# Performance work log

Measured on AMD Instinct MI355X. Metric: run time of the kernel, lower is better.

## Reference

```python
import jax, jax.numpy as jnp
import numpy as np

EMBED_DIM = 1024
NUM_HEADS = 16
MICRO_HEADS = 8
HEAD_DIM = EMBED_DIM // NUM_HEADS
N_BLOCKS = NUM_HEADS // MICRO_HEADS
B, N = 2, 2048


def setup_inputs() -> dict:
    key = jax.random.key(0)
    ks = jax.random.split(key, 9)
    s = 1.0 / np.sqrt(EMBED_DIM)
    return {
        "x": jax.random.normal(ks[0], (B, N, EMBED_DIM), dtype=jnp.float32),
        "Wq": jax.random.uniform(ks[1], (EMBED_DIM, EMBED_DIM), jnp.float32, -s, s),
        "bq": jax.random.uniform(ks[2], (EMBED_DIM,), jnp.float32, -s, s),
        "Wk": jax.random.uniform(ks[3], (EMBED_DIM, EMBED_DIM), jnp.float32, -s, s),
        "bk": jax.random.uniform(ks[4], (EMBED_DIM,), jnp.float32, -s, s),
        "Wv": jax.random.uniform(ks[5], (EMBED_DIM, EMBED_DIM), jnp.float32, -s, s),
        "bv": jax.random.uniform(ks[6], (EMBED_DIM,), jnp.float32, -s, s),
        "Wo": jax.random.uniform(ks[7], (EMBED_DIM, EMBED_DIM), jnp.float32, -s, s),
        "bo": jax.random.uniform(ks[8], (EMBED_DIM,), jnp.float32, -s, s),
    }


def _scramble(t, b, n):
    # Replicates torch's Qh[:, :, hs:he, :].contiguous().view(B*mh, N, dh)
    # which is a raw row-major reshape mixing (N, mh) -> (mh, N) per batch.
    # (B, N, E) -> (B, N, nb, mh, dh) -> (B, nb, N, mh, dh) -> raw reshape -> (B, nb, mh, N, dh)
    t = t.reshape(b, n, N_BLOCKS, MICRO_HEADS, HEAD_DIM)
    t = jnp.transpose(t, (0, 2, 1, 3, 4))
    return t.reshape(b, N_BLOCKS, MICRO_HEADS, n, HEAD_DIM)


def reference(x, Wq, bq, Wk, bk, Wv, bv, Wo, bo):
    b, n, e = x.shape
    scale = HEAD_DIM ** -0.5
    Q = x @ Wq.T + bq
    K = x @ Wk.T + bk
    V = x @ Wv.T + bv
    q = _scramble(Q, b, n)  # (B, nb, mh, N, dh)
    k = _scramble(K, b, n)
    v = _scramble(V, b, n)
    s = jnp.einsum("bgmqd,bgmkd->bgmqk", q, k) * scale  # (B, nb, mh, N, N)
    causal = jnp.tril(jnp.ones((n, n), dtype=bool))
    s = jnp.where(causal, s, -jnp.inf)
    p = jax.nn.softmax(s, axis=-1)
    ctx = jnp.einsum("bgmqk,bgmkd->bgmqd", p, v)  # (B, nb, mh, N, dh)
    # inverse raw reshape: (mh, N, dh) -> (N, mh*dh) per (b, g), then concat blocks
    ctx = ctx.reshape(b, N_BLOCKS, n, MICRO_HEADS * HEAD_DIM)
    ctx = jnp.transpose(ctx, (0, 2, 1, 3)).reshape(b, n, e)
    return ctx @ Wo.T + bo
```

## Files before the change

### kernel.cpp

```cpp
#include <hip/hip_runtime.h>
#include <hip/hip_bf16.h>


typedef unsigned short ushortT;
typedef __attribute__((ext_vector_type(8))) short short8;
typedef __attribute__((ext_vector_type(4))) float floatx4;

__device__ inline float bf2f(ushortT u) {
    union { unsigned int i; float f; } v; v.i = ((unsigned int)u) << 16; return v.f;
}
__device__ inline ushortT f2bf(float f) {
    union { float f; unsigned int i; } v; v.f = f;
    unsigned int x = v.i;
    return (ushortT)((x + 0x7fffu + ((x >> 16) & 1u)) >> 16);
}

__device__ inline void gl_lds16(const ushortT* g, ushortT* lds) {
    __builtin_amdgcn_global_load_lds(
        (const __attribute__((address_space(1))) unsigned int*)g,
        (__attribute__((address_space(3))) unsigned int*)lds, 16, 0, 0);
}

__global__ __launch_bounds__(256) void cvt_bf16(
    const float* __restrict__ x,
    const float* __restrict__ Wq, const float* __restrict__ Wk,
    const float* __restrict__ Wv, const float* __restrict__ Wo,
    ushortT* __restrict__ xb, ushortT* __restrict__ Wb)
{
    const unsigned tid = blockIdx.x * 256 + threadIdx.x;
    const size_t e = (size_t)tid * 8;
    const float* src;
    ushortT* dst;
    size_t off;
    if (e < (size_t)(4u << 20)) { src = x; dst = xb; off = e; }
    else {
        const size_t r = e - (size_t)(4u << 20);
        const int wsel = (int)(r >> 20);
        off = r & 0xFFFFFu;
        src = (wsel == 0) ? Wq : (wsel == 1) ? Wk : (wsel == 2) ? Wv : Wo;
        dst = Wb + ((size_t)wsel << 20);
    }
    const float4 f0 = ((const float4*)(src + off))[0];
    const float4 f1 = ((const float4*)(src + off))[1];
    union { __hip_bfloat162 h[4]; uint4 u; } pk;
    pk.h[0] = __float22bfloat162_rn(float2{f0.x, f0.y});
    pk.h[1] = __float22bfloat162_rn(float2{f0.z, f0.w});
    pk.h[2] = __float22bfloat162_rn(float2{f1.x, f1.y});
    pk.h[3] = __float22bfloat162_rn(float2{f1.z, f1.w});
    *(uint4*)(dst + off) = pk.u;
}

template <bool OUT_F32>
__global__ __launch_bounds__(256) void gemm_lds(
    const ushortT* __restrict__ A, const ushortT* __restrict__ Wst,
    const float* __restrict__ b0, const float* __restrict__ b1, const float* __restrict__ b2,
    void* __restrict__ O0, void* __restrict__ O1, void* __restrict__ O2)
{
    __shared__ __align__(16) ushortT As[128 * 64];
    __shared__ __align__(16) ushortT Bs[128 * 64];
    const int t = threadIdx.x;
    const int m0 = blockIdx.y * 128;
    const int n0g = blockIdx.x * 128;
    const int mat = n0g >> 10;
    const int n0 = n0g & 1023;
    const ushortT* W = Wst + ((size_t)mat << 20);
    const float* bias = (mat == 0) ? b0 : (mat == 1) ? b1 : b2;
    void* Out        = (mat == 0) ? O0 : (mat == 1) ? O1 : O2;

    const int w = t >> 6, lane = t & 63;
    const int wm = w >> 1, wn = w & 1;
    const int col16 = lane & 15, quad = lane >> 4;

    floatx4 acc[4][4];
    for (int i = 0; i < 4; i++)
        for (int j = 0; j < 4; j++) acc[i][j] = (floatx4)0.0f;

    const int cid0 = w * 256 + lane;

    for (int k0 = 0; k0 < 1024; k0 += 64) {
        #pragma unroll
        for (int q = 0; q < 4; q++) {
            const int cid = cid0 + q * 64;
            const int row = cid >> 3;
            const int sch = (cid & 7) ^ (row & 7);
            ushortT* dstA = As + (size_t)(w * 256 + q * 64) * 8;
            ushortT* dstB = Bs + (size_t)(w * 256 + q * 64) * 8;
            gl_lds16(A + (size_t)(m0 + row) * 1024 + k0 + sch * 8, dstA);
            gl_lds16(W + (size_t)(n0 + row) * 1024 + k0 + sch * 8, dstB);
        }
        __syncthreads();
        #pragma unroll
        for (int ks = 0; ks < 64; ks += 32) {
            const int cbase = (ks >> 3) + quad;
            const int sw = col16 & 7;
            short8 a[4], b[4];
            #pragma unroll
            for (int i = 0; i < 4; i++) {
                const int row = wm * 64 + i * 16 + col16;
                a[i] = *(const short8*)(As + row * 64 + ((cbase ^ sw) << 3));
            }
            #pragma unroll
            for (int j = 0; j < 4; j++) {
                const int row = wn * 64 + j * 16 + col16;
                b[j] = *(const short8*)(Bs + row * 64 + ((cbase ^ sw) << 3));
            }
            #pragma unroll
            for (int i = 0; i < 4; i++)
                #pragma unroll
                for (int j = 0; j < 4; j++)
                    acc[i][j] = __builtin_amdgcn_mfma_f32_16x16x32_bf16(b[j], a[i], acc[i][j], 0, 0, 0);
        }
        __syncthreads();
    }

    #pragma unroll
    for (int i = 0; i < 4; i++) {
        const int m = m0 + wm * 64 + i * 16 + col16;
        #pragma unroll
        for (int j = 0; j < 4; j++) {
            const int nb = n0 + wn * 64 + j * 16 + quad * 4;
            const float4 bv4 = *(const float4*)(bias + nb);
            const float v0 = acc[i][j][0] + bv4.x;
            const float v1 = acc[i][j][1] + bv4.y;
            const float v2 = acc[i][j][2] + bv4.z;
            const float v3 = acc[i][j][3] + bv4.w;
            if constexpr (OUT_F32) {
                *(float4*)((float*)Out + (size_t)m * 1024 + nb) = float4{v0, v1, v2, v3};
            } else {
                union { __hip_bfloat162 h[2]; unsigned long long u; } pk2;
                pk2.h[0] = __float22bfloat162_rn(float2{v0, v1});
                pk2.h[1] = __float22bfloat162_rn(float2{v2, v3});
                *(unsigned long long*)((ushortT*)Out + (size_t)m * 1024 + nb) = pk2.u;
            }
        }
    }
}

__global__ __launch_bounds__(256) void transpose_v(
    const ushortT* __restrict__ Vb, ushortT* __restrict__ VT)
{
    __shared__ ushortT L[64 * 65];
    const int bid = blockIdx.x;
    const int pt = bid & 31, s = bid >> 5;
    const int bb = s >> 4, g = (s >> 3) & 1, mh = s & 7;
    const size_t baseoff = (size_t)bb * 2048 * 1024 + (size_t)g * 512;
    const int t = threadIdx.x;
    {
        const int pr = t >> 2, seg = t & 3;
        const int i = mh * 2048 + pt * 64 + pr;
        const uint4* src = (const uint4*)(Vb + baseoff + (size_t)(i >> 3) * 1024 + (i & 7) * 64 + seg * 16);
        union { uint4 u[2]; ushortT h[16]; } tmp;
        tmp.u[0] = src[0]; tmp.u[1] = src[1];
        #pragma unroll
        for (int d = 0; d < 16; d++) L[pr * 65 + seg * 16 + d] = tmp.h[d];
    }
    __syncthreads();
    {
        const int dc = t >> 2, pseg = t & 3;
        union { uint4 u[2]; ushortT h[16]; } tmp;
        #pragma unroll
        for (int j = 0; j < 16; j++) tmp.h[j] = L[(pseg * 16 + j) * 65 + dc];
        uint4* dst = (uint4*)(VT + (size_t)s * 64 * 2048 + (size_t)dc * 2048 + pt * 64 + pseg * 16);
        dst[0] = tmp.u[0]; dst[1] = tmp.u[1];
    }
}

__global__ __launch_bounds__(256) void attn(
    const ushortT* __restrict__ Qb, const ushortT* __restrict__ Kb,
    const ushortT* __restrict__ VT, ushortT* __restrict__ Cb)
{
    __shared__ __align__(16) ushortT Ks[2][64 * 64];
    __shared__ __align__(16) ushortT Vs[2][64 * 64];
    __shared__ __align__(16) ushortT Ps[64 * 64];

    const int t = threadIdx.x;
    const int bid = blockIdx.x;
    const int xcd = bid & 7;
    const int jj  = bid >> 3;
    const int s   = xcd * 4 + (jj >> 4);
    const int p   = jj & 15;
    const int qtA = p, qtB = 31 - p;
    const int bb = s >> 4, g = (s >> 3) & 1, mh = s & 7;

    const int w = t >> 6, lane = t & 63;
    const int col16 = lane & 15, quad = lane >> 4;

    const size_t baseoff = (size_t)bb * 2048 * 1024 + (size_t)g * 512;
    const size_t vtbase  = (size_t)s * 64 * 2048;
    const int i0A = mh * 2048 + qtA * 64;
    const int i0B = mh * 2048 + qtB * 64;
    const int qloc = w * 16 + col16;
    const int psw = qloc & 7;
    const float KL = 0.125f * 1.44269504f;

    short8 qreg[2][2];
    {
        const int iA = i0A + qloc, iB = i0B + qloc;
        const ushortT* pA = Qb + baseoff + (size_t)(iA >> 3) * 1024 + (iA & 7) * 64;
        const ushortT* pB = Qb + baseoff + (size_t)(iB >> 3) * 1024 + (iB & 7) * 64;
        qreg[0][0] = *(const short8*)(pA + quad * 8);
        qreg[0][1] = *(const short8*)(pA + 32 + quad * 8);
        qreg[1][0] = *(const short8*)(pB + quad * 8);
        qreg[1][1] = *(const short8*)(pB + 32 + quad * 8);
    }

    auto stageKV = [&](int kt, int bsel) {
        ushortT* kd = &Ks[bsel][0] + (size_t)(w * 128) * 8;
        ushortT* vd = &Vs[bsel][0] + (size_t)(w * 128) * 8;
        #pragma unroll
        for (int q = 0; q < 2; q++) {
            const int cid = w * 128 + q * 64 + lane;
            const int row = cid >> 3;
            const int sch = (cid & 7) ^ (row & 7);
            const int jr = mh * 2048 + kt * 64 + row;
            gl_lds16(Kb + baseoff + (size_t)(jr >> 3) * 1024 + (jr & 7) * 64 + sch * 8,
                     kd + q * 64 * 8);
            gl_lds16(VT + vtbase + (size_t)row * 2048 + kt * 64 + sch * 8,
                     vd + q * 64 * 8);
        }
    };

    float l_s[2] = {0.f, 0.f};
    floatx4 Oacc[2][4];
    for (int tl = 0; tl < 2; tl++)
        for (int c = 0; c < 4; c++) Oacc[tl][c] = (floatx4)0.0f;

    stageKV(0, 0);
    const int ktmax = qtB;
    for (int kt = 0; kt <= ktmax; ++kt) {
        const int bsel = kt & 1;
        __syncthreads();
        if (kt < ktmax) stageKV(kt + 1, bsel ^ 1);

        #pragma unroll
        for (int tile = 0; tile < 2; ++tile) {
            const int qt = tile ? qtB : qtA;
            if (kt > qt) continue;

            floatx4 sc[4];
            for (int c = 0; c < 4; c++) sc[c] = (floatx4)0.0f;
            #pragma unroll
            for (int ks = 0; ks < 64; ks += 32) {
                const short8 bq = qreg[tile][ks >> 5];
                #pragma unroll
                for (int c = 0; c < 4; c++) {
                    const int krow = c * 16 + col16;
                    const short8 ak = *(const short8*)(&Ks[bsel][0] + krow * 64 +
                                        ((((ks >> 3) + quad) ^ (krow & 7)) << 3));
                    sc[c] = __builtin_amdgcn_mfma_f32_16x16x32_bf16(ak, bq, sc[c], 0, 0, 0);
                }
            }

            if (kt == qt) {
                #pragma unroll
                for (int c = 0; c < 4; c++)
                    #pragma unroll
                    for (int r = 0; r < 4; r++)
                        if ((c * 16 + quad * 4 + r) > qloc) sc[c][r] = -1e30f;
            }

            float lsum = l_s[tile];
            #pragma unroll
            for (int c = 0; c < 4; c++) {
                #pragma unroll
                for (int r = 0; r < 4; r++) {
                    const float pv = exp2f(sc[c][r] * KL);
                    sc[c][r] = pv;
                    lsum += pv;
                }
                const int key0 = c * 16 + quad * 4;
                union { __hip_bfloat162 h[2]; unsigned long long u; } pk2;
                pk2.h[0] = __float22bfloat162_rn(float2{sc[c][0], sc[c][1]});
                pk2.h[1] = __float22bfloat162_rn(float2{sc[c][2], sc[c][3]});
                *(unsigned long long*)(Ps + qloc * 64 +
                    (((key0 >> 3) ^ psw) << 3) + (key0 & 7)) = pk2.u;
            }
            l_s[tile] = lsum;

            #pragma unroll
            for (int kk = 0; kk < 64; kk += 32) {
                const short8 bp = *(const short8*)(Ps + qloc * 64 +
                                    ((((kk >> 3) + quad) ^ psw) << 3));
                #pragma unroll
                for (int c = 0; c < 4; c++) {
                    const int drow = c * 16 + col16;
                    const short8 av = *(const short8*)(&Vs[bsel][0] + drow * 64 +
                                        ((((kk >> 3) + quad) ^ (drow & 7)) << 3));
                    Oacc[tile][c] = __builtin_amdgcn_mfma_f32_16x16x32_bf16(av, bp, Oacc[tile][c], 0, 0, 0);
                }
            }
        }
    }

    l_s[0] += __shfl_xor(l_s[0], 16); l_s[0] += __shfl_xor(l_s[0], 32);
    l_s[1] += __shfl_xor(l_s[1], 16); l_s[1] += __shfl_xor(l_s[1], 32);

    #pragma unroll
    for (int tile = 0; tile < 2; ++tile) {
        const int i = (tile ? i0B : i0A) + qloc;
        const float inv = 1.0f / l_s[tile];
        ushortT* dst = Cb + baseoff + (size_t)(i >> 3) * 1024 + (i & 7) * 64;
        #pragma unroll
        for (int c = 0; c < 4; c++) {
            union { __hip_bfloat162 h[2]; unsigned long long u; } pk2;
            pk2.h[0] = __float22bfloat162_rn(float2{Oacc[tile][c][0] * inv, Oacc[tile][c][1] * inv});
            pk2.h[1] = __float22bfloat162_rn(float2{Oacc[tile][c][2] * inv, Oacc[tile][c][3] * inv});
            *(unsigned long long*)(dst + c * 16 + quad * 4) = pk2.u;
        }
    }
}

extern "C" void kernel_launch(void* const* d_in, const int* in_sizes, int n_in,
                              void* d_out, int out_size, void* d_ws, size_t ws_size,
                              hipStream_t stream)
{
    const float* x  = (const float*)d_in[0];
    const float* Wq = (const float*)d_in[1];
    const float* bq = (const float*)d_in[2];
    const float* Wk = (const float*)d_in[3];
    const float* bk = (const float*)d_in[4];
    const float* Wv = (const float*)d_in[5];
    const float* bv = (const float*)d_in[6];
    const float* Wo = (const float*)d_in[7];
    const float* bo = (const float*)d_in[8];

    const size_t M1 = (size_t)1024 * 1024;
    ushortT* Wb  = (ushortT*)d_ws;
    ushortT* xb  = Wb + 4 * M1;
    ushortT* Qb  = xb + 4 * M1;
    ushortT* Kb  = Qb + 4 * M1;
    ushortT* Vb  = (ushortT*)d_out;
    ushortT* VTb = xb;
    ushortT* Cb  = Qb;

    dim3 blk(256);
    cvt_bf16<<<dim3(4096), blk, 0, stream>>>(x, Wq, Wk, Wv, Wo, xb, Wb);
    gemm_lds<false><<<dim3(24, 32), blk, 0, stream>>>(
        xb, Wb, bq, bk, bv, Qb, Kb, Vb);
    transpose_v<<<dim3(1024), blk, 0, stream>>>(Vb, VTb);
    attn<<<dim3(512), blk, 0, stream>>>(Qb, Kb, VTb, Cb);
    gemm_lds<true><<<dim3(8, 32), blk, 0, stream>>>(
        Cb, Wb + 3 * M1, bo, bo, bo, d_out, d_out, d_out);
}
```

Baseline: 212.3 us.

## Split attention into one q-tile per block and halve output GEMM N-tile

Attention blocks previously handled a balanced pair of query tiles (p and 31-p) that shared the K/V stream. Each block now handles a single query tile, so the grid doubles to 1024 blocks, with a zigzag mapping that spreads long and short causal tiles across the launch order. Separately, the output projection GEMM gains a 64-wide N-tile variant, doubling its grid to 512 blocks to fill more CUs. The trade-off is more redundant K/V loads and less work per block, in return for more parallelism and less per-block register pressure.

```diff
diff --git a/kernel.cpp b/kernel.cpp
--- a/kernel.cpp
+++ b/kernel.cpp
@@ -50,17 +50,20 @@
     *(uint4*)(dst + off) = pk.u;
 }
 
-template <bool OUT_F32>
+template <bool OUT_F32, bool N64>
 __global__ __launch_bounds__(256) void gemm_lds(
     const ushortT* __restrict__ A, const ushortT* __restrict__ Wst,
     const float* __restrict__ b0, const float* __restrict__ b1, const float* __restrict__ b2,
     void* __restrict__ O0, void* __restrict__ O1, void* __restrict__ O2)
 {
+    constexpr int NT = N64 ? 64 : 128;
+    constexpr int NJ = N64 ? 2 : 4;
+    constexpr int WQ = N64 ? 2 : 4;
     __shared__ __align__(16) ushortT As[128 * 64];
-    __shared__ __align__(16) ushortT Bs[128 * 64];
+    __shared__ __align__(16) ushortT Bs[NT * 64];
     const int t = threadIdx.x;
     const int m0 = blockIdx.y * 128;
-    const int n0g = blockIdx.x * 128;
+    const int n0g = blockIdx.x * NT;
     const int mat = n0g >> 10;
     const int n0 = n0g & 1023;
     const ushortT* W = Wst + ((size_t)mat << 20);
@@ -71,43 +74,49 @@
     const int wm = w >> 1, wn = w & 1;
     const int col16 = lane & 15, quad = lane >> 4;
 
-    floatx4 acc[4][4];
+    floatx4 acc[4][NJ];
     for (int i = 0; i < 4; i++)
-        for (int j = 0; j < 4; j++) acc[i][j] = (floatx4)0.0f;
-
-    const int cid0 = w * 256 + lane;
+        for (int j = 0; j < NJ; j++) acc[i][j] = (floatx4)0.0f;
+
+    const int cid0 = w * (N64 ? 128 : 256) + lane;
 
     for (int k0 = 0; k0 < 1024; k0 += 64) {
         #pragma unroll
         for (int q = 0; q < 4; q++) {
+            const int cid = w * 256 + q * 64 + lane;
+            const int row = cid >> 3;
+            const int sch = (cid & 7) ^ (row & 7);
+            gl_lds16(A + (size_t)(m0 + row) * 1024 + k0 + sch * 8,
+                     As + (size_t)(w * 256 + q * 64) * 8);
+        }
+        #pragma unroll
+        for (int q = 0; q < WQ; q++) {
             const int cid = cid0 + q * 64;
             const int row = cid >> 3;
             const int sch = (cid & 7) ^ (row & 7);
-            ushortT* dstA = As + (size_t)(w * 256 + q * 64) * 8;
-            ushortT* dstB = Bs + (size_t)(w * 256 + q * 64) * 8;
-            gl_lds16(A + (size_t)(m0 + row) * 1024 + k0 + sch * 8, dstA);
-            gl_lds16(W + (size_t)(n0 + row) * 1024 + k0 + sch * 8, dstB);
+            gl_lds16(W + (size_t)(n0 + row) * 1024 + k0 + sch * 8,
+                     Bs + (size_t)(w * (N64 ? 128 : 256) + q * 64) * 8);
         }
         __syncthreads();
         #pragma unroll
         for (int ks = 0; ks < 64; ks += 32) {
             const int cbase = (ks >> 3) + quad;
             const int sw = col16 & 7;
-            short8 a[4], b[4];
+            short8 a[4], b[NJ];
             #pragma unroll
             for (int i = 0; i < 4; i++) {
                 const int row = wm * 64 + i * 16 + col16;
                 a[i] = *(const short8*)(As + row * 64 + ((cbase ^ sw) << 3));
             }
             #pragma unroll
-            for (int j = 0; j < 4; j++) {
-                const int row = wn * 64 + j * 16 + col16;
+            for (int j = 0; j < NJ; j++) {
+                const int row = wn * (NT / 2) + j * 16 + col16;
                 b[j] = *(const short8*)(Bs + row * 64 + ((cbase ^ sw) << 3));
             }
             #pragma unroll
             for (int i = 0; i < 4; i++)
                 #pragma unroll
-                for (int j = 0; j < 4; j++)
+                for (int j = 0; j < NJ; j++)
                     acc[i][j] = __builtin_amdgcn_mfma_f32_16x16x32_bf16(b[j], a[i], acc[i][j], 0, 0, 0);
         }
         __syncthreads();
@@ -117,8 +126,8 @@
     for (int i = 0; i < 4; i++) {
         const int m = m0 + wm * 64 + i * 16 + col16;
         #pragma unroll
-        for (int j = 0; j < 4; j++) {
-            const int nb = n0 + wn * 64 + j * 16 + quad * 4;
+        for (int j = 0; j < NJ; j++) {
+            const int nb = n0 + wn * (NT / 2) + j * 16 + quad * 4;
             const float4 bv4 = *(const float4*)(bias + nb);
             const float v0 = acc[i][j][0] + bv4.x;
             const float v1 = acc[i][j][1] + bv4.y;
@@ -176,10 +185,11 @@
     const int t = threadIdx.x;
     const int bid = blockIdx.x;
     const int xcd = bid & 7;
-    const int jj  = bid >> 3;
-    const int s   = xcd * 4 + (jj >> 4);
-    const int p   = jj & 15;
-    const int qtA = p, qtB = 31 - p;
+    const int u = bid >> 3;
+    const int s = xcd * 4 + (u & 3);
+    const int x5 = u >> 2;
+    const int qt = (x5 < 8) ? x5 : (x5 < 16) ? (39 - x5)
+                 : (x5 < 24) ? (x5 - 8) : (47 - x5);
     const int bb = s >> 4, g = (s >> 3) & 1, mh = s & 7;
 
     const int w = t >> 6, lane = t & 63;
@@ -187,21 +197,17 @@
 
     const size_t baseoff = (size_t)bb * 2048 * 1024 + (size_t)g * 512;
     const size_t vtbase  = (size_t)s * 64 * 2048;
-    const int i0A = mh * 2048 + qtA * 64;
-    const int i0B = mh * 2048 + qtB * 64;
+    const int i0 = mh * 2048 + qt * 64;
     const int qloc = w * 16 + col16;
     const int psw = qloc & 7;
     const float KL = 0.125f * 1.44269504f;
 
-    short8 qreg[2][2];
+    short8 qreg[2];
     {
-        const int iA = i0A + qloc, iB = i0B + qloc;
-        const ushortT* pA = Qb + baseoff + (size_t)(iA >> 3) * 1024 + (iA & 7) * 64;
-        const ushortT* pB = Qb + baseoff + (size_t)(iB >> 3) * 1024 + (iB & 7) * 64;
-        qreg[0][0] = *(const short8*)(pA + quad * 8);
-        qreg[0][1] = *(const short8*)(pA + 32 + quad * 8);
-        qreg[1][0] = *(const short8*)(pB + quad * 8);
-        qreg[1][1] = *(const short8*)(pB + 32 + quad * 8);
+        const int i = i0 + qloc;
+        const ushortT* p = Qb + baseoff + (size_t)(i >> 3) * 1024 + (i & 7) * 64;
+        qreg[0] = *(const short8*)(p + quad * 8);
+        qreg[1] = *(const short8*)(p + 32 + quad * 8);
     }
 
     auto stageKV = [&](int kt, int bsel) {
@@ -220,91 +226,82 @@
         }
     };
 
-    float l_s[2] = {0.f, 0.f};
-    floatx4 Oacc[2][4];
-    for (int tl = 0; tl < 2; tl++)
-        for (int c = 0; c < 4; c++) Oacc[tl][c] = (floatx4)0.0f;
+    float l_s = 0.f;
+    floatx4 Oacc[4];
+    for (int c = 0; c < 4; c++) Oacc[c] = (floatx4)0.0f;
 
     stageKV(0, 0);
-    const int ktmax = qtB;
-    for (int kt = 0; kt <= ktmax; ++kt) {
+    for (int kt = 0; kt <= qt; ++kt) {
         const int bsel = kt & 1;
         __syncthreads();
-        if (kt < ktmax) stageKV(kt + 1, bsel ^ 1);
-
-        #pragma unroll
-        for (int tile = 0; tile < 2; ++tile) {
-            const int qt = tile ? qtB : qtA;
-            if (kt > qt) continue;
-
-            floatx4 sc[4];
-            for (int c = 0; c < 4; c++) sc[c] = (floatx4)0.0f;
-            #pragma unroll
-            for (int ks = 0; ks < 64; ks += 32) {
-                const short8 bq = qreg[tile][ks >> 5];
+        if (kt < qt) stageKV(kt + 1, bsel ^ 1);
+
+        floatx4 sc[4];
+        for (int c = 0; c < 4; c++) sc[c] = (floatx4)0.0f;
+        #pragma unroll
+        for (int ks = 0; ks < 64; ks += 32) {
+            const short8 bq = qreg[ks >> 5];
+            #pragma unroll
+            for (int c = 0; c < 4; c++) {
+                const int krow = c * 16 + col16;
+                const short8 ak = *(const short8*)(&Ks[bsel][0] + krow * 64 +
+                                    ((((ks >> 3) + quad) ^ (krow & 7)) << 3));
+                sc[c] = __builtin_amdgcn_mfma_f32_16x16x32_bf16(ak, bq, sc[c], 0, 0, 0);
+            }
+        }
+
+        if (kt == qt) {
+            #pragma unroll
+            for (int c = 0; c < 4; c++)
                 #pragma unroll
-                for (int c = 0; c < 4; c++) {
-                    const int krow = c * 16 + col16;
-                    const short8 ak = *(const short8*)(&Ks[bsel][0] + krow * 64 +
-                                        ((((ks >> 3) + quad) ^ (krow & 7)) << 3));
-                    sc[c] = __builtin_amdgcn_mfma_f32_16x16x32_bf16(ak, bq, sc[c], 0, 0, 0);
-                }
-            }
-
-            if (kt == qt) {
-                #pragma unroll
-                for (int c = 0; c < 4; c++)
-                    #pragma unroll
-                    for (int r = 0; r < 4; r++)
-                        if ((c * 16 + quad * 4 + r) > qloc) sc[c][r] = -1e30f;
-            }
-
-            float lsum = l_s[tile];
+                for (int r = 0; r < 4; r++)
+                    if ((c * 16 + quad * 4 + r) > qloc) sc[c][r] = -1e30f;
+        }
+
+        float lsum = l_s;
+        #pragma unroll
+        for (int c = 0; c < 4; c++) {
+            #pragma unroll
+            for (int r = 0; r < 4; r++) {
+                const float pv = exp2f(sc[c][r] * KL);
+                sc[c][r] = pv;
+                lsum += pv;
+            }
+            const int key0 = c * 16 + quad * 4;
+            union { __hip_bfloat162 h[2]; unsigned long long u; } pk2;
+            pk2.h[0] = __float22bfloat162_rn(float2{sc[c][0], sc[c][1]});
+            pk2.h[1] = __float22bfloat162_rn(float2{sc[c][2], sc[c][3]});
+            *(unsigned long long*)(Ps + qloc * 64 +
+                (((key0 >> 3) ^ psw) << 3) + (key0 & 7)) = pk2.u;
+        }
+        l_s = lsum;
+
+        #pragma unroll
+        for (int kk = 0; kk < 64; kk += 32) {
+            const short8 bp = *(const short8*)(Ps + qloc * 64 +
+                                ((((kk >> 3) + quad) ^ psw) << 3));
             #pragma unroll
             for (int c = 0; c < 4; c++) {
-                #pragma unroll
-                for (int r = 0; r < 4; r++) {
-                    const float pv = exp2f(sc[c][r] * KL);
-                    sc[c][r] = pv;
-                    lsum += pv;
-                }
-                const int key0 = c * 16 + quad * 4;
-                union { __hip_bfloat162 h[2]; unsigned long long u; } pk2;
-                pk2.h[0] = __float22bfloat162_rn(float2{sc[c][0], sc[c][1]});
-                pk2.h[1] = __float22bfloat162_rn(float2{sc[c][2], sc[c][3]});
-                *(unsigned long long*)(Ps + qloc * 64 +
-                    (((key0 >> 3) ^ psw) << 3) + (key0 & 7)) = pk2.u;
-            }
-            l_s[tile] = lsum;
-
-            #pragma unroll
-            for (int kk = 0; kk < 64; kk += 32) {
-                const short8 bp = *(const short8*)(Ps + qloc * 64 +
-                                    ((((kk >> 3) + quad) ^ psw) << 3));
-                #pragma unroll
-                for (int c = 0; c < 4; c++) {
-                    const int drow = c * 16 + col16;
-                    const short8 av = *(const short8*)(&Vs[bsel][0] + drow * 64 +
-                                        ((((kk >> 3) + quad) ^ (drow & 7)) << 3));
-                    Oacc[tile][c] = __builtin_amdgcn_mfma_f32_16x16x32_bf16(av, bp, Oacc[tile][c], 0, 0, 0);
-                }
-            }
-        }
-    }
-
-    l_s[0] += __shfl_xor(l_s[0], 16); l_s[0] += __shfl_xor(l_s[0], 32);
-    l_s[1] += __shfl_xor(l_s[1], 16); l_s[1] += __shfl_xor(l_s[1], 32);
-
-    #pragma unroll
-    for (int tile = 0; tile < 2; ++tile) {
-        const int i = (tile ? i0B : i0A) + qloc;
-        const float inv = 1.0f / l_s[tile];
+                const int drow = c * 16 + col16;
+                const short8 av = *(const short8*)(&Vs[bsel][0] + drow * 64 +
+                                    ((((kk >> 3) + quad) ^ (drow & 7)) << 3));
+                Oacc[c] = __builtin_amdgcn_mfma_f32_16x16x32_bf16(av, bp, Oacc[c], 0, 0, 0);
+            }
+        }
+    }
+
+    l_s += __shfl_xor(l_s, 16);
+    l_s += __shfl_xor(l_s, 32);
+
+    {
+        const int i = i0 + qloc;
+        const float inv = 1.0f / l_s;
         ushortT* dst = Cb + baseoff + (size_t)(i >> 3) * 1024 + (i & 7) * 64;
         #pragma unroll
         for (int c = 0; c < 4; c++) {
             union { __hip_bfloat162 h[2]; unsigned long long u; } pk2;
-            pk2.h[0] = __float22bfloat162_rn(float2{Oacc[tile][c][0] * inv, Oacc[tile][c][1] * inv});
-            pk2.h[1] = __float22bfloat162_rn(float2{Oacc[tile][c][2] * inv, Oacc[tile][c][3] * inv});
+            pk2.h[0] = __float22bfloat162_rn(float2{Oacc[c][0] * inv, Oacc[c][1] * inv});
+            pk2.h[1] = __float22bfloat162_rn(float2{Oacc[c][2] * inv, Oacc[c][3] * inv});
             *(unsigned long long*)(dst + c * 16 + quad * 4) = pk2.u;
         }
     }
@@ -335,10 +332,10 @@
 
     dim3 blk(256);
     cvt_bf16<<<dim3(4096), blk, 0, stream>>>(x, Wq, Wk, Wv, Wo, xb, Wb);
-    gemm_lds<false><<<dim3(24, 32), blk, 0, stream>>>(
+    gemm_lds<false, false><<<dim3(24, 32), blk, 0, stream>>>(
         xb, Wb, bq, bk, bv, Qb, Kb, Vb);
     transpose_v<<<dim3(1024), blk, 0, stream>>>(Vb, VTb);
-    attn<<<dim3(512), blk, 0, stream>>>(Qb, Kb, VTb, Cb);
-    gemm_lds<true><<<dim3(8, 32), blk, 0, stream>>>(
+    attn<<<dim3(1024), blk, 0, stream>>>(Qb, Kb, VTb, Cb);
+    gemm_lds<true, true><<<dim3(16, 32), blk, 0, stream>>>(
         Cb, Wb + 3 * M1, bo, bo, bo, d_out, d_out, d_out);
 }
```

Measured after the change: 204.3 us. -3.8%, faster.
